# Kernel optimization log

Hardware: AMD Instinct MI355X
Metric: run time of the kernel (lower is better)

## Reference

```python
import jax, jax.numpy as jnp
import numpy as np

N_SRC, N_MID, N_DST = 200000, 40000, 8000
R = 4
E1, E2 = 1000000, 200000
IN_F, HID_F, OUT_F = 256, 128, 128


def setup_inputs() -> dict:
    key = jax.random.key(0)
    ks = jax.random.split(key, 10)
    x = jax.random.normal(ks[0], (N_SRC, IN_F), dtype=jnp.float32)
    W1 = jax.random.normal(ks[1], (R, IN_F, HID_F), dtype=jnp.float32) * 0.05
    b1 = jax.random.normal(ks[2], (R, HID_F), dtype=jnp.float32) * 0.05
    W2 = jax.random.normal(ks[3], (R, HID_F, OUT_F), dtype=jnp.float32) * 0.05
    b2 = jax.random.normal(ks[4], (R, OUT_F), dtype=jnp.float32) * 0.05
    src1 = jax.random.randint(ks[5], (R, E1), 0, N_SRC, dtype=jnp.int32)
    dst1 = jax.random.randint(ks[6], (R, E1), 0, N_MID, dtype=jnp.int32)
    src2 = jax.random.randint(ks[7], (R, E2), 0, N_MID, dtype=jnp.int32)
    dst2 = jax.random.randint(ks[8], (R, E2), 0, N_DST, dtype=jnp.int32)
    return {"x": x, "W1": W1, "b1": b1, "W2": W2, "b2": b2,
            "src1": src1, "dst1": dst1, "src2": src2, "dst2": dst2}


def _hetero_graphconv(h_src, W, b, src, dst, n_dst):
    """Sum over relations of GraphConv(norm='right'):
    per relation r: agg = scatter_add(dst, (h_src @ W[r])[src]); out_r = agg / in_deg + b[r]."""
    n_rel = W.shape[0]
    out = jnp.zeros((n_dst, W.shape[-1]), dtype=h_src.dtype)
    for r in range(n_rel):  # small fixed relation count
        m = h_src @ W[r]                                    # [N_src, F_out] (transform first: F_in >= F_out)
        msg = m[src[r]]                                     # [E, F_out] gather
        agg = jax.ops.segment_sum(msg, dst[r], num_segments=n_dst)
        deg = jax.ops.segment_sum(jnp.ones((src.shape[1],), dtype=h_src.dtype),
                                  dst[r], num_segments=n_dst)
        norm = jnp.where(deg > 0, 1.0 / deg, 0.0)           # norm='right', zero-degree -> 0
        out = out + agg * norm[:, None] + b[r]
    return out


def reference(x, W1, b1, W2, b2, src1, dst1, src2, dst2):
    h = _hetero_graphconv(x, W1, b1, src1, dst1, N_MID)     # layer 1 -> [N_MID, HID_F]
    out = _hetero_graphconv(h, W2, b2, src2, dst2, N_DST)   # layer 2 -> [N_DST, OUT_F]
    return out
```

## Files before the change

### kernel.cpp

```cpp
#include <hip/hip_runtime.h>
#include <hip/hip_bf16.h>

#define N_SRC  200000
#define N_MIDN 40000
#define N_DSTN 8000
#define RREL   4
#define E1N    1000000
#define E2N    200000
#define CAP    96
#define EPB    8192
#define NB1C   123
#define NB2C   25
#define NPAD2  8064

typedef __attribute__((ext_vector_type(8))) short bf16x8;
typedef __attribute__((ext_vector_type(4))) float f32x4;
typedef __attribute__((ext_vector_type(4))) unsigned short u16x4;

__device__ __forceinline__ unsigned short f2bf(float f) {
    unsigned int u = __float_as_uint(f);
    u = (u + 0x7FFFu + ((u >> 16) & 1u)) >> 16;
    return (unsigned short)u;
}

__device__ __forceinline__ float bflo(unsigned int u) { return __uint_as_float(u << 16); }
__device__ __forceinline__ float bfhi(unsigned int u) { return __uint_as_float(u & 0xFFFF0000u); }

__device__ __forceinline__ void gload_lds16(const void* g, void* l) {
    __builtin_amdgcn_global_load_lds((const __attribute__((address_space(1))) void*)g,
                                     (__attribute__((address_space(3))) void*)l, 16, 0, 0);
}

__global__ __launch_bounds__(256) void count_kernel(
    const int* __restrict__ dst, unsigned char* __restrict__ rank8,
    unsigned int* __restrict__ hist, int epr, int ndst4, int nb)
{
    __shared__ unsigned int cnt4[10240];
    const int r = blockIdx.y, b = blockIdx.x;
    for (int i = threadIdx.x; i < ndst4; i += 256) cnt4[i] = 0;
    __syncthreads();
    const int e0 = b * EPB;
    const int ne = min(EPB, epr - e0);
    const int* dp = dst + (size_t)r * epr + e0;
    unsigned char* rp = rank8 + (size_t)r * epr + e0;
    for (int i = threadIdx.x; i < ne; i += 256) {
        int d = dp[i];
        unsigned int sh = (d & 3) * 8;
        unsigned int old = atomicAdd(&cnt4[d >> 2], 1u << sh);
        rp[i] = (unsigned char)((old >> sh) & 0xFFu);
    }
    __syncthreads();
    unsigned int* hp = hist + ((size_t)r * nb + b) * ndst4;
    for (int i = threadIdx.x; i < ndst4; i += 256) hp[i] = cnt4[i];
}

__global__ __launch_bounds__(256) void scan_kernel(
    unsigned int* __restrict__ hist, int* __restrict__ cnt,
    int ndst, int ndst4, int nb)
{
    int id = blockIdx.x * 256 + threadIdx.x;
    if (id >= RREL * ndst) return;
    int r = id / ndst;
    int node = id - r * ndst;
    unsigned char* hb = (unsigned char*)hist;
    const size_t stride = (size_t)ndst4 * 4;
    unsigned char* p0 = hb + (size_t)r * nb * stride + node;
    unsigned int run = 0;
    for (int b = 0; b < nb; ++b) {
        unsigned char* pp = p0 + (size_t)b * stride;
        unsigned int c = *pp;
        *pp = (unsigned char)run;
        run += c;
    }
    cnt[id] = (int)run;
}

template<int K>
__global__ __launch_bounds__(256) void convwf_kernel(
    const float* __restrict__ W, unsigned short* __restrict__ WtF)
{
    constexpr int KS = K / 32;
    int id = blockIdx.x * 256 + threadIdx.x;
    if (id >= RREL * KS * 8 * 64) return;
    int lane = id & 63;
    int fi   = id >> 6;
    int nblk = fi & 7;
    int rk   = fi >> 3;
    int kki  = rk & (KS - 1);
    int rr   = rk / KS;
    int n  = nblk * 16 + (lane & 15);
    int k0 = kki * 32 + (lane >> 4) * 8;
    unsigned short* op = WtF + (size_t)id * 8;
    #pragma unroll
    for (int j = 0; j < 8; ++j)
        op[j] = f2bf(W[((size_t)(rr * K + k0 + j)) * 128 + n]);
}

__global__ __launch_bounds__(512, 4) void fused_kernel(
    const float* __restrict__ X,
    const unsigned short* __restrict__ WtF,
    unsigned short* __restrict__ Mout, int M, int nscat,
    const int* __restrict__ src1, const int* __restrict__ dst1,
    const unsigned char* __restrict__ rank81, const unsigned int* __restrict__ hist1,
    int* __restrict__ ell1,
    const int* __restrict__ src2, const int* __restrict__ dst2,
    const unsigned char* __restrict__ rank82, const unsigned int* __restrict__ hist2,
    int* __restrict__ ell2)
{
    __shared__ char lds[40960];
    const int bid = blockIdx.x;
    const int tid = threadIdx.x;

    if (bid < nscat) {
        int sb = bid;
        const int* src; const int* dst; const unsigned char* rank8;
        const unsigned int* hist; int* ell; int epr, ndst4, nb, r, b;
        if (sb < 4 * NB1C) {
            r = sb / NB1C; b = sb - r * NB1C;
            src = src1; dst = dst1; rank8 = rank81; hist = hist1; ell = ell1;
            epr = E1N; ndst4 = N_MIDN / 4; nb = NB1C;
        } else {
            sb -= 4 * NB1C;
            r = sb / NB2C; b = sb - r * NB2C;
            src = src2; dst = dst2; rank8 = rank82; hist = hist2; ell = ell2;
            epr = E2N; ndst4 = N_DSTN / 4; nb = NB2C;
        }
        unsigned int* pre4 = (unsigned int*)lds;
        const unsigned int* hp = hist + ((size_t)r * nb + b) * ndst4;
        for (int i = tid; i < ndst4; i += 512) pre4[i] = hp[i];
        __syncthreads();
        const int e0 = b * EPB;
        const int ne = min(EPB, epr - e0);
        const size_t eb = (size_t)r * epr + e0;
        const unsigned char* pre = (const unsigned char*)pre4;
        const int ndst = ndst4 * 4;
        for (int i = tid; i < ne; i += 512) {
            int d = dst[eb + i];
            int s = src[eb + i];
            int slot = (int)rank8[eb + i] + (int)pre[d];
            if (slot < CAP) ell[((size_t)r * ndst + d) * CAP + slot] = s;
        }
        return;
    }

    unsigned short* As = (unsigned short*)lds;
    const int m0 = (bid - nscat) * 64;

    #pragma unroll
    for (int jj = 0; jj < 2; ++jj) {
        float4 v[4];
        #pragma unroll
        for (int j = 0; j < 4; ++j) {
            int slot = jj * 2048 + j * 512 + tid;
            int row = slot >> 6, col4 = slot & 63;
            int grow = m0 + row; if (grow >= M) grow = M - 1;
            v[j] = *(const float4*)&X[(size_t)grow * 256 + col4 * 4];
        }
        #pragma unroll
        for (int j = 0; j < 4; ++j) {
            int slot = jj * 2048 + j * 512 + tid;
            int row = slot >> 6, col4 = slot & 63;
            int h   = col4 >> 5, c4l = col4 & 31;
            u16x4 o;
            o.x = f2bf(v[j].x); o.y = f2bf(v[j].y);
            o.z = f2bf(v[j].z); o.w = f2bf(v[j].w);
            int bb  = c4l * 8;
            int off = (((bb >> 4) ^ (row & 7)) << 4) | (bb & 15);
            *(u16x4*)((char*)As + h * 16384 + row * 256 + off) = o;
        }
    }
    __syncthreads();

    const int lane = tid & 63;
    const int wave = tid >> 6;
    const int r    = wave & 3;
    const int nh   = (wave >> 2) & 1;
    const int wn   = nh * 64;
    const int lr   = lane & 15;
    const int kg   = lane >> 4;
    const int xorv = (lr & 7) << 4;
    const unsigned short* Wr = WtF + (size_t)r * 8 * 8 * 512;

    f32x4 acc[4][4] = {};
    #pragma unroll
    for (int h = 0; h < 2; ++h) {
        const char* Ap = (const char*)As + h * 16384;
        #pragma unroll
        for (int ks = 0; ks < 4; ++ks) {
            bf16x8 af[4], bv[4];
            const int kb = (ks * 64 + kg * 16) ^ xorv;
            #pragma unroll
            for (int mi = 0; mi < 4; ++mi)
                af[mi] = *(const bf16x8*)(Ap + (mi * 16 + lr) * 256 + kb);
            const int kk32 = h * 4 + ks;
            #pragma unroll
            for (int ni = 0; ni < 4; ++ni)
                bv[ni] = *(const bf16x8*)&Wr[((size_t)kk32 * 8 + nh * 4 + ni) * 512 + lane * 8];
            #pragma unroll
            for (int mi = 0; mi < 4; ++mi)
                #pragma unroll
                for (int ni = 0; ni < 4; ++ni)
                    acc[mi][ni] = __builtin_amdgcn_mfma_f32_16x16x32_bf16(
                        af[mi], bv[ni], acc[mi][ni], 0, 0, 0);
        }
    }

    const int rowoff = (lane >> 4) * 4;
    #pragma unroll
    for (int mi = 0; mi < 4; ++mi) {
        #pragma unroll
        for (int j = 0; j < 4; ++j) {
            int grow = m0 + mi * 16 + rowoff + j;
            if (grow < M) {
                #pragma unroll
                for (int ni = 0; ni < 4; ++ni)
                    Mout[(size_t)grow * 512 + r * 128 + wn + ni * 16 + lr]
                        = f2bf(acc[mi][ni][j]);
            }
        }
    }
}

__global__ __launch_bounds__(256) void gather1_kernel(
    const unsigned short* __restrict__ Mt,
    const int* __restrict__ ell, const int* __restrict__ cnt,
    const float* __restrict__ bias,
    unsigned short* __restrict__ outp, int ndst)
{
    __shared__ float red[RREL][2][128];
    const int node = blockIdx.x;
    const int lane = threadIdx.x & 63;
    const int r    = threadIdx.x >> 6;
    const int half = lane >> 5;
    const int sub  = lane & 31;
    const int idx  = r * ndst + node;
    const int c    = cnt[idx];
    const int deg  = c < CAP ? c : CAP;
    const int base = idx * CAP;
    const int coff = r * 128 + sub * 4;

    float a0 = 0.f, a1 = 0.f, a2 = 0.f, a3 = 0.f;
    int e = 0;
    for (; e + 8 <= deg; e += 8) {
        int4 sa = *(const int4*)&ell[base + e];
        int4 sb = *(const int4*)&ell[base + e + 4];
        int sA = half ? sa.y : sa.x;
        int sB = half ? sa.w : sa.z;
        int sC = half ? sb.y : sb.x;
        int sD = half ? sb.w : sb.z;
        uint2 v0 = *(const uint2*)&Mt[(size_t)sA * 512 + coff];
        uint2 v1 = *(const uint2*)&Mt[(size_t)sB * 512 + coff];
        uint2 v2 = *(const uint2*)&Mt[(size_t)sC * 512 + coff];
        uint2 v3 = *(const uint2*)&Mt[(size_t)sD * 512 + coff];
        a0 += bflo(v0.x) + bflo(v1.x) + bflo(v2.x) + bflo(v3.x);
        a1 += bfhi(v0.x) + bfhi(v1.x) + bfhi(v2.x) + bfhi(v3.x);
        a2 += bflo(v0.y) + bflo(v1.y) + bflo(v2.y) + bflo(v3.y);
        a3 += bfhi(v0.y) + bfhi(v1.y) + bfhi(v2.y) + bfhi(v3.y);
    }
    for (; e < deg; e += 2) {
        int s0 = ell[base + e];
        int s1 = (e + 1 < deg) ? ell[base + e + 1] : -1;
        int s = half ? s1 : s0;
        if (s >= 0) {
            uint2 v = *(const uint2*)&Mt[(size_t)s * 512 + coff];
            a0 += bflo(v.x); a1 += bfhi(v.x);
            a2 += bflo(v.y); a3 += bfhi(v.y);
        }
    }
    float norm = c > 0 ? 1.0f / (float)c : 0.0f;
    red[r][half][sub * 4 + 0] = a0 * norm;
    red[r][half][sub * 4 + 1] = a1 * norm;
    red[r][half][sub * 4 + 2] = a2 * norm;
    red[r][half][sub * 4 + 3] = a3 * norm;
    __syncthreads();

    const int t = threadIdx.x;
    if (t < 128) {
        float s = red[0][0][t] + red[0][1][t] + red[1][0][t] + red[1][1][t]
                + red[2][0][t] + red[2][1][t] + red[3][0][t] + red[3][1][t]
                + bias[t] + bias[128 + t] + bias[256 + t] + bias[384 + t];
        outp[(size_t)node * 128 + t] = f2bf(s);
    }
}

__global__ __launch_bounds__(256) void gather2h_kernel(
    const unsigned short* __restrict__ H,
    const int* __restrict__ ell, const int* __restrict__ cnt,
    unsigned short* __restrict__ agg2, int ndst)
{
    __shared__ float red[RREL][2][128];
    const int node = blockIdx.x;
    const int lane = threadIdx.x & 63;
    const int r    = threadIdx.x >> 6;
    const int half = lane >> 5;
    const int sub  = lane & 31;
    const int idx  = r * ndst + node;
    const int c    = cnt[idx];
    const int deg  = c < CAP ? c : CAP;
    const int base = idx * CAP;
    const int coff = sub * 4;

    float a0 = 0.f, a1 = 0.f, a2 = 0.f, a3 = 0.f;
    int e = 0;
    for (; e + 8 <= deg; e += 8) {
        int4 sa = *(const int4*)&ell[base + e];
        int4 sb = *(const int4*)&ell[base + e + 4];
        int sA = half ? sa.y : sa.x;
        int sB = half ? sa.w : sa.z;
        int sC = half ? sb.y : sb.x;
        int sD = half ? sb.w : sb.z;
        uint2 v0 = *(const uint2*)&H[(size_t)sA * 128 + coff];
        uint2 v1 = *(const uint2*)&H[(size_t)sB * 128 + coff];
        uint2 v2 = *(const uint2*)&H[(size_t)sC * 128 + coff];
        uint2 v3 = *(const uint2*)&H[(size_t)sD * 128 + coff];
        a0 += bflo(v0.x) + bflo(v1.x) + bflo(v2.x) + bflo(v3.x);
        a1 += bfhi(v0.x) + bfhi(v1.x) + bfhi(v2.x) + bfhi(v3.x);
        a2 += bflo(v0.y) + bflo(v1.y) + bflo(v2.y) + bflo(v3.y);
        a3 += bfhi(v0.y) + bfhi(v1.y) + bfhi(v2.y) + bfhi(v3.y);
    }
    for (; e < deg; e += 2) {
        int s0 = ell[base + e];
        int s1 = (e + 1 < deg) ? ell[base + e + 1] : -1;
        int s = half ? s1 : s0;
        if (s >= 0) {
            uint2 v = *(const uint2*)&H[(size_t)s * 128 + coff];
            a0 += bflo(v.x); a1 += bfhi(v.x);
            a2 += bflo(v.y); a3 += bfhi(v.y);
        }
    }
    float norm = c > 0 ? 1.0f / (float)c : 0.0f;
    red[r][half][sub * 4 + 0] = a0 * norm;
    red[r][half][sub * 4 + 1] = a1 * norm;
    red[r][half][sub * 4 + 2] = a2 * norm;
    red[r][half][sub * 4 + 3] = a3 * norm;
    __syncthreads();

    const int t  = threadIdx.x;
    const int tt = t & 127;
    const int swz = ((((tt >> 3) ^ (node & 7)) << 3) | (tt & 7));
    #pragma unroll
    for (int q = 0; q < 2; ++q) {
        int rr = (t >> 7) + q * 2;
        float val = red[rr][0][tt] + red[rr][1][tt];
        agg2[((size_t)rr * NPAD2 + node) * 128 + swz] = f2bf(val);
    }
}

__global__ __launch_bounds__(256, 1) void gemm2p_kernel(
    const unsigned short* __restrict__ agg2,
    const unsigned short* __restrict__ WtF,
    const float* __restrict__ b2,
    float* __restrict__ outp, int M)
{
    __shared__ unsigned short As[4 * 128 * 128];

    const int m0  = blockIdx.x * 128;
    const int tid = threadIdx.x;

    #pragma unroll
    for (int rr = 0; rr < 4; ++rr) {
        #pragma unroll
        for (int j = 0; j < 8; ++j) {
            int L = j * 4096 + tid * 16;
            int row  = L >> 8;
            int boff = L & 255;
            gload_lds16((const char*)agg2 + ((size_t)rr * NPAD2 + m0 + row) * 256 + boff,
                        (char*)As + rr * 32768 + L);
        }
    }
    __syncthreads();

    const int lane = tid & 63;
    const int wave = tid >> 6;
    const int mh   = wave & 1;
    const int nh   = wave >> 1;
    const int wm   = mh * 64;
    const int wn   = nh * 64;
    const int lr   = lane & 15;
    const int kg   = lane >> 4;
    const int xorv = (lr & 7) << 4;

    f32x4 acc[4][4] = {};
    #pragma unroll
    for (int rr = 0; rr < 4; ++rr) {
        const char* Ap = (const char*)As + rr * 32768;
        const unsigned short* Wr = WtF + (size_t)rr * 4 * 8 * 512;
        #pragma unroll
        for (int ks = 0; ks < 4; ++ks) {
            bf16x8 af[4], bv[4];
            const int kb = (ks * 64 + kg * 16) ^ xorv;
            #pragma unroll
            for (int mi = 0; mi < 4; ++mi)
                af[mi] = *(const bf16x8*)(Ap + (wm + mi * 16 + lr) * 256 + kb);
            #pragma unroll
            for (int ni = 0; ni < 4; ++ni)
                bv[ni] = *(const bf16x8*)&Wr[((size_t)ks * 8 + nh * 4 + ni) * 512 + lane * 8];
            #pragma unroll
            for (int mi = 0; mi < 4; ++mi)
                #pragma unroll
                for (int ni = 0; ni < 4; ++ni)
                    acc[mi][ni] = __builtin_amdgcn_mfma_f32_16x16x32_bf16(
                        af[mi], bv[ni], acc[mi][ni], 0, 0, 0);
        }
    }

    const int rowoff = (lane >> 4) * 4;
    float bsum[4];
    #pragma unroll
    for (int ni = 0; ni < 4; ++ni) {
        int col = wn + ni * 16 + lr;
        bsum[ni] = b2[col] + b2[128 + col] + b2[256 + col] + b2[384 + col];
    }
    #pragma unroll
    for (int mi = 0; mi < 4; ++mi) {
        #pragma unroll
        for (int j = 0; j < 4; ++j) {
            int grow = m0 + wm + mi * 16 + rowoff + j;
            if (grow < M) {
                #pragma unroll
                for (int ni = 0; ni < 4; ++ni)
                    outp[(size_t)grow * 128 + wn + ni * 16 + lr]
                        = acc[mi][ni][j] + bsum[ni];
            }
        }
    }
}

extern "C" void kernel_launch(void* const* d_in, const int* in_sizes, int n_in,
                              void* d_out, int out_size, void* d_ws, size_t ws_size,
                              hipStream_t stream)
{
    const float* x  = (const float*)d_in[0];
    const float* W1 = (const float*)d_in[1];
    const float* b1 = (const float*)d_in[2];
    const float* W2 = (const float*)d_in[3];
    const float* b2 = (const float*)d_in[4];
    const int* src1 = (const int*)d_in[5];
    const int* dst1 = (const int*)d_in[6];
    const int* src2 = (const int*)d_in[7];
    const int* dst2 = (const int*)d_in[8];

    char* p = (char*)d_ws;
    auto alloc = [&](size_t bytes) {
        char* q = p; p += (bytes + 255) & ~(size_t)255; return q;
    };
    unsigned short* m1    = (unsigned short*)alloc((size_t)N_SRC * 512 * 2);
    int*            ell1  = (int*)alloc((size_t)RREL * N_MIDN * CAP * 4);
    int*            cnt1  = (int*)alloc((size_t)RREL * N_MIDN * 4);
    unsigned short* h     = (unsigned short*)alloc((size_t)N_MIDN * 128 * 2);
    unsigned short* wt1   = (unsigned short*)alloc((size_t)RREL * 8 * 8 * 64 * 8 * 2);
    unsigned short* wt2   = (unsigned short*)alloc((size_t)RREL * 4 * 8 * 64 * 8 * 2);
    unsigned int*   hist1 = (unsigned int*)alloc((size_t)NB1C * RREL * (N_MIDN / 4) * 4);
    unsigned char*  rank81= (unsigned char*)alloc((size_t)RREL * E1N);
    unsigned int*   hist2 = (unsigned int*)alloc((size_t)NB2C * RREL * (N_DSTN / 4) * 4);
    unsigned char*  rank82= (unsigned char*)alloc((size_t)RREL * E2N);
    int*            ell2  = (int*)alloc((size_t)RREL * N_DSTN * CAP * 4);
    int*            cnt2  = (int*)alloc((size_t)RREL * N_DSTN * 4);
    unsigned short* agg2  = (unsigned short*)m1;

    convwf_kernel<256><<<64, 256, 0, stream>>>(W1, wt1);
    convwf_kernel<128><<<32, 256, 0, stream>>>(W2, wt2);

    count_kernel<<<dim3(NB1C, RREL), 256, 0, stream>>>(dst1, rank81, hist1, E1N, N_MIDN / 4, NB1C);
    count_kernel<<<dim3(NB2C, RREL), 256, 0, stream>>>(dst2, rank82, hist2, E2N, N_DSTN / 4, NB2C);
    scan_kernel<<<(RREL * N_MIDN + 255) / 256, 256, 0, stream>>>(hist1, cnt1, N_MIDN, N_MIDN / 4, NB1C);
    scan_kernel<<<(RREL * N_DSTN + 255) / 256, 256, 0, stream>>>(hist2, cnt2, N_DSTN, N_DSTN / 4, NB2C);

    const int NSCAT = 4 * NB1C + 4 * NB2C;
    const int NGEMM = (N_SRC + 63) / 64;
    fused_kernel<<<NSCAT + NGEMM, 512, 0, stream>>>(
        x, wt1, m1, N_SRC, NSCAT,
        src1, dst1, rank81, hist1, ell1,
        src2, dst2, rank82, hist2, ell2);

    gather1_kernel<<<N_MIDN, 256, 0, stream>>>(m1, ell1, cnt1, b1, h, N_MIDN);

    gather2h_kernel<<<N_DSTN, 256, 0, stream>>>(h, ell2, cnt2, agg2, N_DSTN);
    gemm2p_kernel<<<(N_DSTN + 127) / 128, 256, 0, stream>>>(agg2, wt2, b2, (float*)d_out, N_DSTN);
}
```

Measured before the change: 489.9 us.

## Pre-convert X to swizzled bf16 in count kernel, DMA-load tiles in GEMM

Merges the two count kernels into one launch and adds blocks that convert X from fp32 to a pre-swizzled bf16 buffer. The layer-1 GEMM then loads 128-row tiles straight into LDS with global_load_lds, and two blocks share each tile, each covering two relations. This moves fp32 conversion out of the GEMM and halves the bytes it reads. The cost is an extra X round trip through memory, a larger LDS footprint (64KB) and duplicate A-tile loads across the two relation-pair blocks, which may lower occupancy.

```diff
diff --git a/kernel.cpp b/kernel.cpp
--- a/kernel.cpp
+++ b/kernel.cpp
@@ -31,27 +31,60 @@
                                      (__attribute__((address_space(3))) void*)l, 16, 0, 0);
 }
 
-__global__ __launch_bounds__(256) void count_kernel(
-    const int* __restrict__ dst, unsigned char* __restrict__ rank8,
-    unsigned int* __restrict__ hist, int epr, int ndst4, int nb)
+__global__ __launch_bounds__(256) void fusedpre_kernel(
+    const int* __restrict__ dst1, unsigned char* __restrict__ rank81,
+    unsigned int* __restrict__ hist1,
+    const int* __restrict__ dst2, unsigned char* __restrict__ rank82,
+    unsigned int* __restrict__ hist2,
+    const float* __restrict__ X, unsigned short* __restrict__ xb)
 {
     __shared__ unsigned int cnt4[10240];
-    const int r = blockIdx.y, b = blockIdx.x;
-    for (int i = threadIdx.x; i < ndst4; i += 256) cnt4[i] = 0;
-    __syncthreads();
-    const int e0 = b * EPB;
-    const int ne = min(EPB, epr - e0);
-    const int* dp = dst + (size_t)r * epr + e0;
-    unsigned char* rp = rank8 + (size_t)r * epr + e0;
-    for (int i = threadIdx.x; i < ne; i += 256) {
-        int d = dp[i];
-        unsigned int sh = (d & 3) * 8;
-        unsigned int old = atomicAdd(&cnt4[d >> 2], 1u << sh);
-        rp[i] = (unsigned char)((old >> sh) & 0xFFu);
-    }
-    __syncthreads();
-    unsigned int* hp = hist + ((size_t)r * nb + b) * ndst4;
-    for (int i = threadIdx.x; i < ndst4; i += 256) hp[i] = cnt4[i];
+    const int bid = blockIdx.x;
+    const int tid = threadIdx.x;
+    const int NCNT = 4 * NB1C + 4 * NB2C;
+
+    if (bid < NCNT) {
+        const int* dst; unsigned char* rank8; unsigned int* hist;
+        int epr, ndst4, nb, r, b, sb = bid;
+        if (sb < 4 * NB1C) {
+            r = sb / NB1C; b = sb - r * NB1C;
+            dst = dst1; rank8 = rank81; hist = hist1;
+            epr = E1N; ndst4 = N_MIDN / 4; nb = NB1C;
+        } else {
+            sb -= 4 * NB1C;
+            r = sb / NB2C; b = sb - r * NB2C;
+            dst = dst2; rank8 = rank82; hist = hist2;
+            epr = E2N; ndst4 = N_DSTN / 4; nb = NB2C;
+        }
+        for (int i = tid; i < ndst4; i += 256) cnt4[i] = 0;
+        __syncthreads();
+        const int e0 = b * EPB;
+        const int ne = min(EPB, epr - e0);
+        const int* dp = dst + (size_t)r * epr + e0;
+        unsigned char* rp = rank8 + (size_t)r * epr + e0;
+        for (int i = tid; i < ne; i += 256) {
+            int d = dp[i];
+            unsigned int sh = (d & 3) * 8;
+            unsigned int old = atomicAdd(&cnt4[d >> 2], 1u << sh);
+            rp[i] = (unsigned char)((old >> sh) & 0xFFu);
+        }
+        __syncthreads();
+        unsigned int* hp = hist + ((size_t)r * nb + b) * ndst4;
+        for (int i = tid; i < ndst4; i += 256) hp[i] = cnt4[i];
+        return;
+    }
+
+    int id  = (bid - NCNT) * 256 + tid;
+    int row = id >> 5;
+    int c   = id & 31;
+    const float4* xp = (const float4*)(X + ((size_t)row << 8) + (c << 3));
+    float4 va = xp[0], vb = xp[1];
+    u16x4 o0, o1;
+    o0.x = f2bf(va.x); o0.y = f2bf(va.y); o0.z = f2bf(va.z); o0.w = f2bf(va.w);
+    o1.x = f2bf(vb.x); o1.y = f2bf(vb.y); o1.z = f2bf(vb.z); o1.w = f2bf(vb.w);
+    int cs = c ^ (row & 7);
+    u16x4* op = (u16x4*)(xb + ((size_t)row << 8) + (cs << 3));
+    op[0] = o0; op[1] = o1;
 }
 
 __global__ __launch_bounds__(256) void scan_kernel(
@@ -96,8 +129,8 @@
         op[j] = f2bf(W[((size_t)(rr * K + k0 + j)) * 128 + n]);
 }
 
-__global__ __launch_bounds__(512, 4) void fused_kernel(
-    const float* __restrict__ X,
+__global__ __launch_bounds__(512, 4) void fusedmain_kernel(
+    const unsigned short* __restrict__ xb,
     const unsigned short* __restrict__ WtF,
     unsigned short* __restrict__ Mout, int M, int nscat,
     const int* __restrict__ src1, const int* __restrict__ dst1,
@@ -107,7 +140,7 @@
     const unsigned char* __restrict__ rank82, const unsigned int* __restrict__ hist2,
     int* __restrict__ ell2)
 {
-    __shared__ char lds[40960];
+    __shared__ char lds[65536];
     const int bid = blockIdx.x;
     const int tid = threadIdx.x;
 
@@ -143,66 +176,49 @@
         return;
     }
 
-    unsigned short* As = (unsigned short*)lds;
-    const int m0 = (bid - nscat) * 64;
-
-    #pragma unroll
-    for (int jj = 0; jj < 2; ++jj) {
-        float4 v[4];
-        #pragma unroll
-        for (int j = 0; j < 4; ++j) {
-            int slot = jj * 2048 + j * 512 + tid;
-            int row = slot >> 6, col4 = slot & 63;
-            int grow = m0 + row; if (grow >= M) grow = M - 1;
-            v[j] = *(const float4*)&X[(size_t)grow * 256 + col4 * 4];
-        }
-        #pragma unroll
-        for (int j = 0; j < 4; ++j) {
-            int slot = jj * 2048 + j * 512 + tid;
-            int row = slot >> 6, col4 = slot & 63;
-            int h   = col4 >> 5, c4l = col4 & 31;
-            u16x4 o;
-            o.x = f2bf(v[j].x); o.y = f2bf(v[j].y);
-            o.z = f2bf(v[j].z); o.w = f2bf(v[j].w);
-            int bb  = c4l * 8;
-            int off = (((bb >> 4) ^ (row & 7)) << 4) | (bb & 15);
-            *(u16x4*)((char*)As + h * 16384 + row * 256 + off) = o;
-        }
+    const int g  = bid - nscat;
+    const int t  = g >> 1;
+    const int pr = g & 1;
+    const int m0 = t * 128;
+
+    const char* gp = (const char*)xb + (size_t)m0 * 512;
+    #pragma unroll
+    for (int j = 0; j < 8; ++j) {
+        int L = j * 8192 + tid * 16;
+        gload_lds16(gp + L, lds + L);
     }
     __syncthreads();
 
     const int lane = tid & 63;
     const int wave = tid >> 6;
-    const int r    = wave & 3;
-    const int nh   = (wave >> 2) & 1;
+    const int rl   = wave & 1;
+    const int nh   = (wave >> 1) & 1;
+    const int mh   = (wave >> 2) & 1;
+    const int rel  = pr * 2 + rl;
+    const int wm   = mh * 64;
     const int wn   = nh * 64;
     const int lr   = lane & 15;
     const int kg   = lane >> 4;
     const int xorv = (lr & 7) << 4;
-    const unsigned short* Wr = WtF + (size_t)r * 8 * 8 * 512;
+    const unsigned short* Wr = WtF + (size_t)rel * 8 * 8 * 512;
 
     f32x4 acc[4][4] = {};
     #pragma unroll
-    for (int h = 0; h < 2; ++h) {
-        const char* Ap = (const char*)As + h * 16384;
-        #pragma unroll
-        for (int ks = 0; ks < 4; ++ks) {
-            bf16x8 af[4], bv[4];
-            const int kb = (ks * 64 + kg * 16) ^ xorv;
-            #pragma unroll
-            for (int mi = 0; mi < 4; ++mi)
-                af[mi] = *(const bf16x8*)(Ap + (mi * 16 + lr) * 256 + kb);
-            const int kk32 = h * 4 + ks;
+    for (int ks = 0; ks < 8; ++ks) {
+        bf16x8 af[4], bv[4];
+        const int kb = (ks * 64 + kg * 16) ^ xorv;
+        #pragma unroll
+        for (int mi = 0; mi < 4; ++mi)
+            af[mi] = *(const bf16x8*)(lds + (wm + mi * 16 + lr) * 512 + kb);
+        #pragma unroll
+        for (int ni = 0; ni < 4; ++ni)
+            bv[ni] = *(const bf16x8*)&Wr[((size_t)ks * 8 + nh * 4 + ni) * 512 + lane * 8];
+        #pragma unroll
+        for (int mi = 0; mi < 4; ++mi)
             #pragma unroll
             for (int ni = 0; ni < 4; ++ni)
-                bv[ni] = *(const bf16x8*)&Wr[((size_t)kk32 * 8 + nh * 4 + ni) * 512 + lane * 8];
-            #pragma unroll
-            for (int mi = 0; mi < 4; ++mi)
-                #pragma unroll
-                for (int ni = 0; ni < 4; ++ni)
-                    acc[mi][ni] = __builtin_amdgcn_mfma_f32_16x16x32_bf16(
-                        af[mi], bv[ni], acc[mi][ni], 0, 0, 0);
-        }
+                acc[mi][ni] = __builtin_amdgcn_mfma_f32_16x16x32_bf16(
+                    af[mi], bv[ni], acc[mi][ni], 0, 0, 0);
     }
 
     const int rowoff = (lane >> 4) * 4;
@@ -210,11 +226,11 @@
     for (int mi = 0; mi < 4; ++mi) {
         #pragma unroll
         for (int j = 0; j < 4; ++j) {
-            int grow = m0 + mi * 16 + rowoff + j;
+            int grow = m0 + wm + mi * 16 + rowoff + j;
             if (grow < M) {
                 #pragma unroll
                 for (int ni = 0; ni < 4; ++ni)
-                    Mout[(size_t)grow * 512 + r * 128 + wn + ni * 16 + lr]
+                    Mout[(size_t)grow * 512 + rel * 128 + wn + ni * 16 + lr]
                         = f2bf(acc[mi][ni][j]);
             }
         }
@@ -274,12 +290,12 @@
     red[r][half][sub * 4 + 3] = a3 * norm;
     __syncthreads();
 
-    const int t = threadIdx.x;
-    if (t < 128) {
-        float s = red[0][0][t] + red[0][1][t] + red[1][0][t] + red[1][1][t]
-                + red[2][0][t] + red[2][1][t] + red[3][0][t] + red[3][1][t]
-                + bias[t] + bias[128 + t] + bias[256 + t] + bias[384 + t];
-        outp[(size_t)node * 128 + t] = f2bf(s);
+    const int tt = threadIdx.x;
+    if (tt < 128) {
+        float s = red[0][0][tt] + red[0][1][tt] + red[1][0][tt] + red[1][1][tt]
+                + red[2][0][tt] + red[2][1][tt] + red[3][0][tt] + red[3][1][tt]
+                + bias[tt] + bias[128 + tt] + bias[256 + tt] + bias[384 + tt];
+        outp[(size_t)node * 128 + tt] = f2bf(s);
     }
 }
 
@@ -445,6 +461,7 @@
         char* q = p; p += (bytes + 255) & ~(size_t)255; return q;
     };
     unsigned short* m1    = (unsigned short*)alloc((size_t)N_SRC * 512 * 2);
+    unsigned short* xb    = (unsigned short*)alloc((size_t)(N_SRC + 64) * 256 * 2);
     int*            ell1  = (int*)alloc((size_t)RREL * N_MIDN * CAP * 4);
     int*            cnt1  = (int*)alloc((size_t)RREL * N_MIDN * 4);
     unsigned short* h     = (unsigned short*)alloc((size_t)N_MIDN * 128 * 2);
@@ -461,15 +478,18 @@
     convwf_kernel<256><<<64, 256, 0, stream>>>(W1, wt1);
     convwf_kernel<128><<<32, 256, 0, stream>>>(W2, wt2);
 
-    count_kernel<<<dim3(NB1C, RREL), 256, 0, stream>>>(dst1, rank81, hist1, E1N, N_MIDN / 4, NB1C);
-    count_kernel<<<dim3(NB2C, RREL), 256, 0, stream>>>(dst2, rank82, hist2, E2N, N_DSTN / 4, NB2C);
+    const int NCNT = 4 * NB1C + 4 * NB2C;
+    const int NCVX = (N_SRC * 32) / 256;
+    fusedpre_kernel<<<NCNT + NCVX, 256, 0, stream>>>(
+        dst1, rank81, hist1, dst2, rank82, hist2, x, xb);
+
     scan_kernel<<<(RREL * N_MIDN + 255) / 256, 256, 0, stream>>>(hist1, cnt1, N_MIDN, N_MIDN / 4, NB1C);
     scan_kernel<<<(RREL * N_DSTN + 255) / 256, 256, 0, stream>>>(hist2, cnt2, N_DSTN, N_DSTN / 4, NB2C);
 
-    const int NSCAT = 4 * NB1C + 4 * NB2C;
-    const int NGEMM = (N_SRC + 63) / 64;
-    fused_kernel<<<NSCAT + NGEMM, 512, 0, stream>>>(
-        x, wt1, m1, N_SRC, NSCAT,
+    const int NSCAT = NCNT;
+    const int NT1   = (N_SRC + 127) / 128;
+    fusedmain_kernel<<<NSCAT + 2 * NT1, 512, 0, stream>>>(
+        xb, wt1, m1, N_SRC, NSCAT,
         src1, dst1, rank81, hist1, ell1,
         src2, dst2, rank82, hist2, ell2);
 
```

After: 527.7 us. 1.08x slower.
